# Performance work log

Hardware: AMD Instinct MI355X
Metric: run time of the kernel (lower is better)

Reference implementation:

```python
import jax, jax.numpy as jnp
import numpy as np

N, H, B, SS = 8192, 128, 64, 20


def _rate(z_a, z_b, k_idx, psi, W_om, b_om):
    # z_a, z_b: [..., H]; k_idx: int [...] event-type selector
    Wsel = W_om[k_idx]                    # [..., 2H]
    bsel = b_om[k_idx]
    psel = psi[k_idx]
    zab = jnp.concatenate([z_a, z_b], -1)
    zba = jnp.concatenate([z_b, z_a], -1)
    g = 0.5 * ((zab * Wsel).sum(-1) + bsel + (zba * Wsel).sum(-1) + bsel)
    x = jnp.clip(g / psel, -75.0, 75.0)
    return psel * jnp.log1p(jnp.exp(x))  # psi * log(1 + exp(g/psi))


def _forward(u, v, t, k, u_others, v_others, A, S, embeddings, last_event_time,
             W_S, W_R, W_t, W_h, b_h, psi, W_om, b_om):
    # 1) event intensities lambda_uvk  [B]
    lam = _rate(embeddings[u], embeddings[v], k, psi, W_om, b_om)
    # 2) survival loss. Replicates the original accumulation (incl. the
    #    v_surv = u_surv + rate_v overwrite bug): L_surv = sum_ev (2*(ru0+ru1)+rv1)/SS, shape [SS]
    z_u = embeddings[u][:, None, :]       # [B,1,H]
    z_v = embeddings[v][:, None, :]
    z_vo = embeddings[v_others]           # [B,SS,H]
    z_uo = embeddings[u_others]
    zub = jnp.broadcast_to(z_u, z_vo.shape)
    zvb = jnp.broadcast_to(z_v, z_uo.shape)
    k0 = jnp.zeros((B, SS), jnp.int32)
    k1 = jnp.ones((B, SS), jnp.int32)
    ru0 = _rate(zub, z_vo, k0, psi, W_om, b_om)
    ru1 = _rate(zub, z_vo, k1, psi, W_om, b_om)
    rv1 = _rate(zvb, z_uo, k1, psi, W_om, b_om)
    L_surv = (2.0 * (ru0 + ru1) + rv1).sum(0) / SS
    # 3) sequential per-event embedding update (the kernel-headroom part)
    def step(carry, ev):
        z, let = carry
        ui, vi, ti = ev
        h = z @ W_h.T + b_h               # [N,H] W_h applied to z_previous
        def side(n1, n2):
            dt = ti - let[n1]
            mask = A[n2] > 0              # neighbors of n2
            q = jnp.exp(S[n2]) * mask
            q = q / (q.sum() + 1e-7)
            vals = jnp.where(mask[:, None], jax.nn.sigmoid(q[:, None] * h), -jnp.inf)
            hs = jnp.where(mask.any(), vals.max(0), 0.0)   # max over neighbors
            return dt, hs
        dt0, hs0 = side(ui, vi)
        dt1, hs1 = side(vi, ui)
        dts = jnp.stack([dt0, dt1])       # [2]
        hstruct = jnp.stack([hs0, hs1])   # [2,H]
        L = hstruct @ W_S.T
        # original indexes z_prev[[n1,n2]] AFTER the inner loop, i.e. [v,u]
        rows = jnp.stack([vi, ui])
        Sterm = z[rows] @ W_R.T
        E = dts[:, None] * W_t[:, 0][None, :]   # Linear(1,H) on time deltas
        z = z.at[rows].set(jax.nn.sigmoid(L + Sterm + E))
        let = let.at[ui].set(ti).at[vi].set(ti)
        return (z, let), None
    (z_final, _), _ = jax.lax.scan(step, (embeddings, last_event_time), (u, v, t))
    return lam, L_surv, z_final


def setup_inputs():
    ks = jax.random.split(jax.random.key(0), 16)
    u = jax.random.randint(ks[0], (B,), 0, N)
    v = jax.random.randint(ks[1], (B,), 0, N)
    t = jnp.sort(jax.random.uniform(ks[2], (B,), jnp.float32) * 100.0)
    k = jax.random.randint(ks[3], (B,), 0, 2)
    u_others = jax.random.randint(ks[4], (B, SS), 0, N)
    v_others = jax.random.randint(ks[5], (B, SS), 0, N)
    Au = jax.random.uniform(ks[6], (N, N)) < (16.0 / N)   # avg degree ~16
    A = jnp.maximum(Au, Au.T).astype(jnp.float32)
    S = A / jnp.clip(A.sum(1, keepdims=True), 1.0)        # degree-normalized init
    embeddings = jax.random.uniform(ks[7], (N, H), jnp.float32)
    last_event_time = jnp.zeros((N,), jnp.float32)
    sc = 1.0 / np.sqrt(H)
    def lin(key, shape, s=sc):
        return jax.random.uniform(key, shape, jnp.float32, -s, s)
    W_S = lin(ks[8], (H, H)); W_R = lin(ks[9], (H, H))
    W_t = lin(ks[10], (H, 1)); W_h = lin(ks[11], (H, H)); b_h = lin(ks[12], (H,))
    psi = 0.5 * jnp.ones((2,), jnp.float32)
    sc2 = 1.0 / np.sqrt(2 * H)
    W_om = jax.random.uniform(ks[13], (2, 2 * H), jnp.float32, -sc2, sc2)
    b_om = jax.random.uniform(ks[14], (2,), jnp.float32, -sc2, sc2)
    return dict(u=u, v=v, t=t, k=k, u_others=u_others, v_others=v_others,
                A=A, S=S, embeddings=embeddings, last_event_time=last_event_time,
                W_S=W_S, W_R=W_R, W_t=W_t, W_h=W_h, b_h=b_h,
                psi=psi, W_om=W_om, b_om=b_om)


def reference(u, v, t, k, u_others, v_others, A, S, embeddings, last_event_time,
              W_S, W_R, W_t, W_h, b_h, psi, W_om, b_om):
    return _forward(u, v, t, k, u_others, v_others, A, S, embeddings, last_event_time,
                    W_S, W_R, W_t, W_h, b_h, psi, W_om, b_om)
```

## Files before the change

### kernel.cpp

```cpp
#include <hip/hip_runtime.h>
#include <math.h>

#define N 8192
#define H 128
#define NEV 64
#define SS 20
#define MAXD 512
#define MAXDIRTY 128
#define RPB 8
#define SPIN_GUARD (1 << 18)

__global__ __launch_bounds__(512) void k_emb(
    const float* __restrict__ emb, const float* __restrict__ W_h,
    const float* __restrict__ b_h, const float* __restrict__ W_om,
    float* __restrict__ h_tab, float* __restrict__ z_out,
    float* __restrict__ d0, float* __restrict__ d1,
    unsigned long long* __restrict__ donebits)
{
    const int tid = threadIdx.x;
    const int c = tid & 127;
    const int s = tid >> 7;
    const int r0 = blockIdx.x * RPB;

    if (blockIdx.x == 0 && tid == 0) donebits[0] = 0ull;

    __shared__ __align__(16) float z4[4 * 128];
    __shared__ float pr[16 * 128];

    float whr[32];
#pragma unroll
    for (int i = 0; i < 32; ++i) whr[i] = W_h[c * H + s * 32 + i];
    const float bh_c = b_h[c];

    const int lane = tid & 63;
    const int wid = tid >> 6;
    const int kof = (wid >= 4) ? 256 : 0;
    const float wk_l = W_om[kof + lane]      + W_om[kof + 128 + lane];
    const float wk_h = W_om[kof + 64 + lane] + W_om[kof + 192 + lane];

    for (int b = 0; b < RPB / 4; ++b) {
        const int rbase = r0 + b * 4;
        __syncthreads();
        const float zv = emb[(size_t)rbase * H + tid];
        z4[tid] = zv;
        z_out[(size_t)rbase * H + tid] = zv;
        __syncthreads();

#pragma unroll
        for (int rr = 0; rr < 4; ++rr) {
            float a = 0.f;
#pragma unroll
            for (int i4 = 0; i4 < 8; ++i4) {
                const float4 zz = *(const float4*)&z4[rr * 128 + s * 32 + i4 * 4];
                a += zz.x * whr[i4 * 4] + zz.y * whr[i4 * 4 + 1] +
                     zz.z * whr[i4 * 4 + 2] + zz.w * whr[i4 * 4 + 3];
            }
            pr[(s * 4 + rr) * 128 + c] = a;
        }
        {
            const int rr = wid & 3;
            float val = z4[rr * 128 + lane] * wk_l + z4[rr * 128 + 64 + lane] * wk_h;
#pragma unroll
            for (int off = 32; off > 0; off >>= 1) val += __shfl_xor(val, off);
            if (lane == 0) {
                if (wid < 4) d0[rbase + rr] = val;
                else         d1[rbase + rr] = val;
            }
        }
        __syncthreads();
        {
            const int rr = s;
            const float h = pr[(0 * 4 + rr) * 128 + c] + pr[(1 * 4 + rr) * 128 + c] +
                            pr[(2 * 4 + rr) * 128 + c] + pr[(3 * 4 + rr) * 128 + c] + bh_c;
            h_tab[(size_t)(rbase + rr) * H + c] = h;
        }
    }
}

__global__ __launch_bounds__(512) void k_parls(
    const int* __restrict__ u, const int* __restrict__ v,
    const float* __restrict__ t, const int* __restrict__ kk,
    const int* __restrict__ u_o, const int* __restrict__ v_o,
    const float* __restrict__ lastt, const float* __restrict__ emb,
    const float* __restrict__ A, const float* __restrict__ S,
    const float* __restrict__ h_tab,
    const float* __restrict__ W_S, const float* __restrict__ W_R,
    const float* __restrict__ W_t, const float* __restrict__ W_h,
    const float* __restrict__ b_h,
    const float* __restrict__ psi, const float* __restrict__ b_om,
    const float* __restrict__ d0, const float* __restrict__ d1,
    float* __restrict__ z_slot, float* __restrict__ h_slot,
    unsigned long long* __restrict__ donebits,
    float* __restrict__ lamout, float* __restrict__ svout,
    float* __restrict__ z_out)
{
    const int bid = blockIdx.x;
    const int tid = threadIdx.x;

    if (bid >= NEV) {
        if (bid == NEV) {
            if (tid < NEV) {
                const int b = tid;
                const int kv = kk[b];
                const float* dk = kv ? d1 : d0;
                const float g = 0.5f * (dk[u[b]] + dk[v[b]]) + b_om[kv];
                const float ps = psi[kv];
                const float x = fminf(75.f, fmaxf(-75.f, g / ps));
                lamout[b] = ps * log1pf(expf(x));
            }
        } else {
            const int s = bid - NEV - 1;
            if (tid < 64) {
                const int b = tid;
                const float p0 = psi[0], p1 = psi[1], bo0 = b_om[0], bo1 = b_om[1];
                const int vo = v_o[b * SS + s], uo = u_o[b * SS + s];
                float g, x;
                g = 0.5f * (d0[u[b]] + d0[vo]) + bo0; x = fminf(75.f, fmaxf(-75.f, g / p0));
                const float ru0 = p0 * log1pf(expf(x));
                g = 0.5f * (d1[u[b]] + d1[vo]) + bo1; x = fminf(75.f, fmaxf(-75.f, g / p1));
                const float ru1 = p1 * log1pf(expf(x));
                g = 0.5f * (d1[v[b]] + d1[uo]) + bo1; x = fminf(75.f, fmaxf(-75.f, g / p1));
                const float rv1 = p1 * log1pf(expf(x));
                float val = 2.f * (ru0 + ru1) + rv1;
#pragma unroll
                for (int off = 32; off > 0; off >>= 1) val += __shfl_xor(val, off);
                if (b == 0) svout[s] = val / (float)SS;
            }
        }
        return;
    }

    const int e = bid;
    const int r = (tid >> 7) & 1;
    const int c = tid & 127;
    const int slot = 2 * e + r;
    const int half = tid >> 8;
    const int ht = tid & 255;

    __shared__ int   uL[NEV], vL[NEV];
    __shared__ int   nbr2[2][MAXD];
    __shared__ float nbe2[2][MAXD];
    __shared__ int   flag2[2][MAXD];
    __shared__ float rs[512];
    __shared__ float redm[512];
    __shared__ float msA[2][128];
    __shared__ int   dlsA[2][MAXDIRTY];
    __shared__ float dlqA[2][MAXDIRTY];
    __shared__ int   dcA[2], degA[2], cntA[2];
    __shared__ float sumA[2];
    __shared__ __align__(16) float hs_s[2][128];
    __shared__ __align__(16) float zz_s[2][128];
    __shared__ __align__(16) float zn_s[2][128];
    __shared__ int   zdepL[2], lastupL[2], nodeL[2];
    __shared__ float dtvL[2];
    __shared__ unsigned long long maskN[4];
    __shared__ unsigned long long maskE[2];
    __shared__ unsigned long long need_s;

    if (tid < NEV)          uL[tid] = u[tid];
    else if (tid < 2 * NEV) vL[tid - NEV] = v[tid - NEV];
    if (tid < 2) { cntA[tid] = 0; dcA[tid] = 0; }
    __syncthreads();

    if (tid < 256) {
        const int i  = tid >> 7;
        const int hj = tid & 127;
        const int lane = tid & 63;
        const int w  = tid >> 6;
        const int node = i ? uL[e] : vL[e];
        const int dtn  = i ? vL[e] : uL[e];
        const bool m1 = (((hj & 1) ? uL[hj >> 1] : vL[hj >> 1]) == node);
        const unsigned long long b1 = __ballot(m1);
        if (lane == 0) maskN[w] = b1;
        const bool m2 = (uL[lane] == dtn) || (vL[lane] == dtn);
        const unsigned long long b2 = __ballot(m2);
        if (lane == 0 && (w & 1) == 0) maskE[i] = b2;
    }
    __syncthreads();
    if (tid < 2) {
        const int i = tid;
        const int sl = 2 * e + i;
        const int dtn = i ? vL[e] : uL[e];
        nodeL[i] = i ? uL[e] : vL[e];
        const unsigned long long lo = maskN[2 * i], hi = maskN[2 * i + 1];
        auto msk = [](int n) -> unsigned long long {
            return (n >= 64) ? ~0ull : ((n <= 0) ? 0ull : ((1ull << n) - 1ull));
        };
        const unsigned long long loB = lo & msk(2 * e);
        const unsigned long long hiB = hi & msk(2 * e - 64);
        int zd = -1;
        if (hiB)      zd = 64 + (63 - __builtin_clzll(hiB));
        else if (loB) zd = 63 - __builtin_clzll(loB);
        zdepL[i] = zd;
        const unsigned long long loA = lo & ~msk(sl + 1);
        const unsigned long long hiA = hi & ~msk(sl + 1 - 64);
        lastupL[i] = ((loA | hiA) == 0ull) ? 1 : 0;
        const unsigned long long me = maskE[i] & msk(e);
        const int pt = me ? (63 - __builtin_clzll(me)) : -1;
        const float lv = (pt >= 0) ? t[pt] : lastt[dtn];
        dtvL[i] = t[e] - lv;
    }
    __syncthreads();

    {
        const int rowN = half ? uL[e] : vL[e];
        const size_t baseN = (size_t)rowN * N;

        float lsum = 0.f;
        {
            const float4* A4 = (const float4*)(A + baseN);
            for (int j4 = ht; j4 < N / 4; j4 += 256) {
                const float4 a4 = A4[j4];
#pragma unroll
                for (int q = 0; q < 4; ++q) {
                    const float av = (q == 0) ? a4.x : (q == 1) ? a4.y
                                   : (q == 2) ? a4.z : a4.w;
                    if (av > 0.f) {
                        const int j = 4 * j4 + q;
                        const float ev = expf(S[baseN + j]);
                        lsum += ev;
                        const int p = atomicAdd(&cntA[half], 1);
                        if (p < MAXD) { nbr2[half][p] = j; nbe2[half][p] = ev; }
                    }
                }
            }
        }
        rs[tid] = lsum;
        __syncthreads();
        for (int off = 128; off > 0; off >>= 1) {
            if (ht < off) rs[tid] += rs[tid + off];
            __syncthreads();
        }
        if (ht == 0) { sumA[half] = rs[tid]; degA[half] = cntA[half]; }
        __syncthreads();

        const int dH = min(cntA[half], MAXD);
        const float rinvH = 1.f / (sumA[half] + 1e-7f);

        for (int j0 = ht; j0 < dH; j0 += 256) {
            const int j = nbr2[half][j0];
            int dep = -1;
            for (int s2 = 2 * e - 1; s2 >= 0; --s2) {
                const int nj = (s2 & 1) ? uL[s2 >> 1] : vL[s2 >> 1];
                if (nj == j) { dep = s2; break; }
            }
            flag2[half][j0] = dep;
        }
        __syncthreads();

        {
            const int cc = ht & 127, pr2 = ht >> 7;
            float m = -INFINITY;
            for (int j0 = pr2; j0 < dH; j0 += 2) {
                if (flag2[half][j0] < 0)
                    m = fmaxf(m, nbe2[half][j0] * rinvH *
                              h_tab[(size_t)nbr2[half][j0] * H + cc]);
            }
            redm[tid] = m;
            __syncthreads();
            if (ht < 128)
                msA[half][cc] = fmaxf(redm[half * 256 + cc],
                                      redm[half * 256 + 128 + cc]);
        }

        for (int j0 = ht; j0 < dH; j0 += 256) {
            const int dep = flag2[half][j0];
            if (dep >= 0) {
                const int p = atomicAdd(&dcA[half], 1);
                if (p < MAXDIRTY) { dlsA[half][p] = dep; dlqA[half][p] = nbe2[half][j0] * rinvH; }
            }
        }
        __syncthreads();
    }

    if (tid == 0) {
        unsigned long long need = 0ull;
        for (int rr = 0; rr < 2; ++rr) {
            const int zd = zdepL[rr];
            if (zd >= 0) need |= 1ull << (zd >> 1);
            const int dn = min(dcA[rr], MAXDIRTY);
            for (int p = 0; p < dn; ++p)
                need |= 1ull << (dlsA[rr][p] >> 1);
        }
        need_s = need;
        if (need) {
            int guard = 0;
            while ((__hip_atomic_load(donebits, __ATOMIC_ACQUIRE,
                                      __HIP_MEMORY_SCOPE_AGENT) & need) != need) {
                __builtin_amdgcn_s_sleep(2);
                if (++guard > SPIN_GUARD) break;
            }
        }
    }
    __syncthreads();
    if (need_s) {
        unsigned long long db = __hip_atomic_load(donebits, __ATOMIC_ACQUIRE,
                                                  __HIP_MEMORY_SCOPE_AGENT);
        (void)db;
    }

    if (tid < 256) {
        float m = msA[r][c];
        const int dn = min(dcA[r], MAXDIRTY);
        for (int p = 0; p < dn; ++p) {
            const int ds = dlsA[r][p];
            const float q = dlqA[r][p];
            m = fmaxf(m, q * h_slot[ds * H + c]);
        }
        hs_s[r][c] = (degA[r] > 0) ? 1.f / (1.f + __expf(-m)) : 0.f;
        const int zd = zdepL[r];
        zz_s[r][c] = (zd >= 0) ? z_slot[zd * H + c]
                               : emb[(size_t)nodeL[r] * H + c];
    }
    __syncthreads();

    if (tid < 256) {
        float g = 0.f;
        const float4* ws4 = (const float4*)(W_S + (size_t)c * H);
        const float4* wr4 = (const float4*)(W_R + (size_t)c * H);
#pragma unroll
        for (int i = 0; i < 32; ++i) {
            const float4 a = ws4[i];
            const float4 b = wr4[i];
            const float4 hh = *(const float4*)&hs_s[r][4 * i];
            const float4 zz = *(const float4*)&zz_s[r][4 * i];
            g += hh.x * a.x + hh.y * a.y + hh.z * a.z + hh.w * a.w +
                 zz.x * b.x + zz.y * b.y + zz.z * b.z + zz.w * b.w;
        }
        g += dtvL[r] * W_t[c];
        const float zv = 1.f / (1.f + __expf(-g));
        zn_s[r][c] = zv;
        z_slot[slot * H + c] = zv;
        if (lastupL[r])
            z_out[(size_t)nodeL[r] * H + c] = zv;
    }
    __syncthreads();

    if (tid < 256) {
        float h = 0.f;
        const float4* wh4 = (const float4*)(W_h + (size_t)c * H);
#pragma unroll
        for (int i = 0; i < 32; ++i) {
            const float4 a = wh4[i];
            const float4 zz = *(const float4*)&zn_s[r][4 * i];
            h += zz.x * a.x + zz.y * a.y + zz.z * a.z + zz.w * a.w;
        }
        h_slot[slot * H + c] = h + b_h[c];
    }

    __syncthreads();
    if (tid == 0) {
        __threadfence();
        __hip_atomic_fetch_or(donebits, 1ull << e, __ATOMIC_RELEASE,
                              __HIP_MEMORY_SCOPE_AGENT);
    }
}

extern "C" void kernel_launch(void* const* d_in, const int* in_sizes, int n_in,
                              void* d_out, int out_size, void* d_ws, size_t ws_size,
                              hipStream_t stream)
{
    const int*   u        = (const int*)d_in[0];
    const int*   v        = (const int*)d_in[1];
    const float* t        = (const float*)d_in[2];
    const int*   k        = (const int*)d_in[3];
    const int*   u_others = (const int*)d_in[4];
    const int*   v_others = (const int*)d_in[5];
    const float* A        = (const float*)d_in[6];
    const float* S        = (const float*)d_in[7];
    const float* emb      = (const float*)d_in[8];
    const float* lastt    = (const float*)d_in[9];
    const float* W_S      = (const float*)d_in[10];
    const float* W_R      = (const float*)d_in[11];
    const float* W_t      = (const float*)d_in[12];
    const float* W_h      = (const float*)d_in[13];
    const float* b_h      = (const float*)d_in[14];
    const float* psi      = (const float*)d_in[15];
    const float* W_om     = (const float*)d_in[16];
    const float* b_om     = (const float*)d_in[17];
    (void)in_sizes; (void)n_in; (void)out_size; (void)ws_size;

    float* wsf    = (float*)d_ws;
    float* h_tab  = wsf;
    float* d0     = h_tab + (size_t)N * H;
    float* d1     = d0 + N;
    float* Mstat  = d1 + N;
    float* dl_q   = Mstat + 128 * H;
    float* z_slot = dl_q + 128 * MAXDIRTY;
    float* h_slot = z_slot + 128 * H;
    int*   deg    = (int*)(h_slot + 128 * H);
    int*   dcnt   = deg + 128;
    int*   dl_s   = dcnt + 128;
    unsigned long long* donebits = (unsigned long long*)(dl_s + 128 * MAXDIRTY);

    float* out    = (float*)d_out;
    float* lamout = out;
    float* svout  = out + NEV;
    float* z_out  = out + NEV + SS;

    k_emb<<<N / RPB, 512, 0, stream>>>(emb, W_h, b_h, W_om, h_tab, z_out,
                                       d0, d1, donebits);
    k_parls<<<NEV + 1 + SS, 512, 0, stream>>>(u, v, t, k, u_others, v_others,
                                              lastt, emb, A, S, h_tab,
                                              W_S, W_R, W_t, W_h, b_h,
                                              psi, b_om, d0, d1,
                                              z_slot, h_slot, donebits,
                                              lamout, svout, z_out);
}
```

Before: 87.03 us.

## Fuse embedding and event kernels into one launch with counter-based dependency

Merges the embedding/h-table kernel and the per-event kernel into one grid. Embedding blocks bump a global atomic counter when they finish. Lambda and survival blocks spin on that counter before reading d0/d1, while the event blocks do their neighbor setup first and wait only before reading h_tab. This overlaps the event preamble with the embedding pass and removes a kernel launch boundary. The rows handled per embedding block are doubled, and a small memset now resets the counters each call. The risks are spin-wait deadlock if the event blocks are scheduled ahead of embedding blocks, and the fact that SPIN_GUARD can break out early, which would leave correctness at risk.

```diff
diff --git a/kernel.cpp b/kernel.cpp
--- a/kernel.cpp
+++ b/kernel.cpp
@@ -7,136 +7,37 @@
 #define SS 20
 #define MAXD 512
 #define MAXDIRTY 128
-#define RPB 8
+#define RPB 16
 #define SPIN_GUARD (1 << 18)
 
-__global__ __launch_bounds__(512) void k_emb(
-    const float* __restrict__ emb, const float* __restrict__ W_h,
-    const float* __restrict__ b_h, const float* __restrict__ W_om,
-    float* __restrict__ h_tab, float* __restrict__ z_out,
-    float* __restrict__ d0, float* __restrict__ d1,
-    unsigned long long* __restrict__ donebits)
-{
-    const int tid = threadIdx.x;
-    const int c = tid & 127;
-    const int s = tid >> 7;
-    const int r0 = blockIdx.x * RPB;
-
-    if (blockIdx.x == 0 && tid == 0) donebits[0] = 0ull;
-
-    __shared__ __align__(16) float z4[4 * 128];
-    __shared__ float pr[16 * 128];
-
-    float whr[32];
-#pragma unroll
-    for (int i = 0; i < 32; ++i) whr[i] = W_h[c * H + s * 32 + i];
-    const float bh_c = b_h[c];
-
-    const int lane = tid & 63;
-    const int wid = tid >> 6;
-    const int kof = (wid >= 4) ? 256 : 0;
-    const float wk_l = W_om[kof + lane]      + W_om[kof + 128 + lane];
-    const float wk_h = W_om[kof + 64 + lane] + W_om[kof + 192 + lane];
-
-    for (int b = 0; b < RPB / 4; ++b) {
-        const int rbase = r0 + b * 4;
-        __syncthreads();
-        const float zv = emb[(size_t)rbase * H + tid];
-        z4[tid] = zv;
-        z_out[(size_t)rbase * H + tid] = zv;
-        __syncthreads();
-
-#pragma unroll
-        for (int rr = 0; rr < 4; ++rr) {
-            float a = 0.f;
-#pragma unroll
-            for (int i4 = 0; i4 < 8; ++i4) {
-                const float4 zz = *(const float4*)&z4[rr * 128 + s * 32 + i4 * 4];
-                a += zz.x * whr[i4 * 4] + zz.y * whr[i4 * 4 + 1] +
-                     zz.z * whr[i4 * 4 + 2] + zz.w * whr[i4 * 4 + 3];
-            }
-            pr[(s * 4 + rr) * 128 + c] = a;
-        }
-        {
-            const int rr = wid & 3;
-            float val = z4[rr * 128 + lane] * wk_l + z4[rr * 128 + 64 + lane] * wk_h;
-#pragma unroll
-            for (int off = 32; off > 0; off >>= 1) val += __shfl_xor(val, off);
-            if (lane == 0) {
-                if (wid < 4) d0[rbase + rr] = val;
-                else         d1[rbase + rr] = val;
-            }
-        }
-        __syncthreads();
-        {
-            const int rr = s;
-            const float h = pr[(0 * 4 + rr) * 128 + c] + pr[(1 * 4 + rr) * 128 + c] +
-                            pr[(2 * 4 + rr) * 128 + c] + pr[(3 * 4 + rr) * 128 + c] + bh_c;
-            h_tab[(size_t)(rbase + rr) * H + c] = h;
-        }
-    }
-}
-
-__global__ __launch_bounds__(512) void k_parls(
+#define EMB_BLOCKS (N / RPB)
+#define LAM_BID    EMB_BLOCKS
+#define SURV_BID0  (LAM_BID + 1)
+#define PAR_BID0   (SURV_BID0 + SS)
+#define GRID_ALL   (PAR_BID0 + NEV)
+#define C_EMB_TARGET EMB_BLOCKS
+
+__global__ __launch_bounds__(512) void k_all(
     const int* __restrict__ u, const int* __restrict__ v,
     const float* __restrict__ t, const int* __restrict__ kk,
     const int* __restrict__ u_o, const int* __restrict__ v_o,
     const float* __restrict__ lastt, const float* __restrict__ emb,
     const float* __restrict__ A, const float* __restrict__ S,
-    const float* __restrict__ h_tab,
     const float* __restrict__ W_S, const float* __restrict__ W_R,
     const float* __restrict__ W_t, const float* __restrict__ W_h,
-    const float* __restrict__ b_h,
+    const float* __restrict__ b_h, const float* __restrict__ W_om,
     const float* __restrict__ psi, const float* __restrict__ b_om,
-    const float* __restrict__ d0, const float* __restrict__ d1,
+    float* __restrict__ h_tab, float* __restrict__ d0, float* __restrict__ d1,
     float* __restrict__ z_slot, float* __restrict__ h_slot,
-    unsigned long long* __restrict__ donebits,
+    unsigned long long* __restrict__ donebits, int* __restrict__ c_emb,
     float* __restrict__ lamout, float* __restrict__ svout,
     float* __restrict__ z_out)
 {
     const int bid = blockIdx.x;
     const int tid = threadIdx.x;
 
-    if (bid >= NEV) {
-        if (bid == NEV) {
-            if (tid < NEV) {
-                const int b = tid;
-                const int kv = kk[b];
-                const float* dk = kv ? d1 : d0;
-                const float g = 0.5f * (dk[u[b]] + dk[v[b]]) + b_om[kv];
-                const float ps = psi[kv];
-                const float x = fminf(75.f, fmaxf(-75.f, g / ps));
-                lamout[b] = ps * log1pf(expf(x));
-            }
-        } else {
-            const int s = bid - NEV - 1;
-            if (tid < 64) {
-                const int b = tid;
-                const float p0 = psi[0], p1 = psi[1], bo0 = b_om[0], bo1 = b_om[1];
-                const int vo = v_o[b * SS + s], uo = u_o[b * SS + s];
-                float g, x;
-                g = 0.5f * (d0[u[b]] + d0[vo]) + bo0; x = fminf(75.f, fmaxf(-75.f, g / p0));
-                const float ru0 = p0 * log1pf(expf(x));
-                g = 0.5f * (d1[u[b]] + d1[vo]) + bo1; x = fminf(75.f, fmaxf(-75.f, g / p1));
-                const float ru1 = p1 * log1pf(expf(x));
-                g = 0.5f * (d1[v[b]] + d1[uo]) + bo1; x = fminf(75.f, fmaxf(-75.f, g / p1));
-                const float rv1 = p1 * log1pf(expf(x));
-                float val = 2.f * (ru0 + ru1) + rv1;
-#pragma unroll
-                for (int off = 32; off > 0; off >>= 1) val += __shfl_xor(val, off);
-                if (b == 0) svout[s] = val / (float)SS;
-            }
-        }
-        return;
-    }
-
-    const int e = bid;
-    const int r = (tid >> 7) & 1;
-    const int c = tid & 127;
-    const int slot = 2 * e + r;
-    const int half = tid >> 8;
-    const int ht = tid & 255;
-
+    __shared__ __align__(16) float z4[4 * 128];
+    __shared__ float pr[16 * 128];
     __shared__ int   uL[NEV], vL[NEV];
     __shared__ int   nbr2[2][MAXD];
     __shared__ float nbe2[2][MAXD];
@@ -156,6 +57,120 @@
     __shared__ unsigned long long maskN[4];
     __shared__ unsigned long long maskE[2];
     __shared__ unsigned long long need_s;
+
+    if (bid < EMB_BLOCKS) {
+        const int c = tid & 127;
+        const int s = tid >> 7;
+        const int r0 = bid * RPB;
+
+        float whr[32];
+#pragma unroll
+        for (int i = 0; i < 32; ++i) whr[i] = W_h[c * H + s * 32 + i];
+        const float bh_c = b_h[c];
+
+        const int lane = tid & 63;
+        const int wid = tid >> 6;
+        const int kof = (wid >= 4) ? 256 : 0;
+        const float wk_l = W_om[kof + lane]      + W_om[kof + 128 + lane];
+        const float wk_h = W_om[kof + 64 + lane] + W_om[kof + 192 + lane];
+
+        for (int b = 0; b < RPB / 4; ++b) {
+            const int rbase = r0 + b * 4;
+            __syncthreads();
+            const float zv = emb[(size_t)rbase * H + tid];
+            z4[tid] = zv;
+            z_out[(size_t)rbase * H + tid] = zv;
+            __syncthreads();
+
+#pragma unroll
+            for (int rr = 0; rr < 4; ++rr) {
+                float a = 0.f;
+#pragma unroll
+                for (int i4 = 0; i4 < 8; ++i4) {
+                    const float4 zz = *(const float4*)&z4[rr * 128 + s * 32 + i4 * 4];
+                    a += zz.x * whr[i4 * 4] + zz.y * whr[i4 * 4 + 1] +
+                         zz.z * whr[i4 * 4 + 2] + zz.w * whr[i4 * 4 + 3];
+                }
+                pr[(s * 4 + rr) * 128 + c] = a;
+            }
+            {
+                const int rr = wid & 3;
+                float val = z4[rr * 128 + lane] * wk_l + z4[rr * 128 + 64 + lane] * wk_h;
+#pragma unroll
+                for (int off = 32; off > 0; off >>= 1) val += __shfl_xor(val, off);
+                if (lane == 0) {
+                    if (wid < 4) d0[rbase + rr] = val;
+                    else         d1[rbase + rr] = val;
+                }
+            }
+            __syncthreads();
+            {
+                const int rr = s;
+                const float h = pr[(0 * 4 + rr) * 128 + c] + pr[(1 * 4 + rr) * 128 + c] +
+                                pr[(2 * 4 + rr) * 128 + c] + pr[(3 * 4 + rr) * 128 + c] + bh_c;
+                h_tab[(size_t)(rbase + rr) * H + c] = h;
+            }
+        }
+        __syncthreads();
+        if (tid == 0) {
+            __threadfence();
+            __hip_atomic_fetch_add(c_emb, 1, __ATOMIC_RELEASE,
+                                   __HIP_MEMORY_SCOPE_AGENT);
+        }
+        return;
+    }
+
+    if (bid < PAR_BID0) {
+        if (tid == 0) {
+            int guard = 0;
+            while (__hip_atomic_load(c_emb, __ATOMIC_ACQUIRE,
+                                     __HIP_MEMORY_SCOPE_AGENT) < C_EMB_TARGET) {
+                __builtin_amdgcn_s_sleep(2);
+                if (++guard > SPIN_GUARD) break;
+            }
+        }
+        __syncthreads();
+        { int x = __hip_atomic_load(c_emb, __ATOMIC_ACQUIRE,
+                                    __HIP_MEMORY_SCOPE_AGENT); (void)x; }
+
+        if (bid == LAM_BID) {
+            if (tid < NEV) {
+                const int b = tid;
+                const int kv = kk[b];
+                const float* dk = kv ? d1 : d0;
+                const float g = 0.5f * (dk[u[b]] + dk[v[b]]) + b_om[kv];
+                const float ps = psi[kv];
+                const float x = fminf(75.f, fmaxf(-75.f, g / ps));
+                lamout[b] = ps * log1pf(expf(x));
+            }
+        } else {
+            const int s = bid - SURV_BID0;
+            if (tid < 64) {
+                const int b = tid;
+                const float p0 = psi[0], p1 = psi[1], bo0 = b_om[0], bo1 = b_om[1];
+                const int vo = v_o[b * SS + s], uo = u_o[b * SS + s];
+                float g, x;
+                g = 0.5f * (d0[u[b]] + d0[vo]) + bo0; x = fminf(75.f, fmaxf(-75.f, g / p0));
+                const float ru0 = p0 * log1pf(expf(x));
+                g = 0.5f * (d1[u[b]] + d1[vo]) + bo1; x = fminf(75.f, fmaxf(-75.f, g / p1));
+                const float ru1 = p1 * log1pf(expf(x));
+                g = 0.5f * (d1[v[b]] + d1[uo]) + bo1; x = fminf(75.f, fmaxf(-75.f, g / p1));
+                const float rv1 = p1 * log1pf(expf(x));
+                float val = 2.f * (ru0 + ru1) + rv1;
+#pragma unroll
+                for (int off = 32; off > 0; off >>= 1) val += __shfl_xor(val, off);
+                if (b == 0) svout[s] = val / (float)SS;
+            }
+        }
+        return;
+    }
+
+    const int e = bid - PAR_BID0;
+    const int r = (tid >> 7) & 1;
+    const int c = tid & 127;
+    const int slot = 2 * e + r;
+    const int half = tid >> 8;
+    const int ht = tid & 255;
 
     if (tid < NEV)          uL[tid] = u[tid];
     else if (tid < 2 * NEV) vL[tid - NEV] = v[tid - NEV];
@@ -247,6 +262,18 @@
             flag2[half][j0] = dep;
         }
         __syncthreads();
+
+        if (tid == 0) {
+            int guard = 0;
+            while (__hip_atomic_load(c_emb, __ATOMIC_ACQUIRE,
+                                     __HIP_MEMORY_SCOPE_AGENT) < C_EMB_TARGET) {
+                __builtin_amdgcn_s_sleep(2);
+                if (++guard > SPIN_GUARD) break;
+            }
+        }
+        __syncthreads();
+        { int x = __hip_atomic_load(c_emb, __ATOMIC_ACQUIRE,
+                                    __HIP_MEMORY_SCOPE_AGENT); (void)x; }
 
         {
             const int cc = ht & 127, pr2 = ht >> 7;
@@ -380,30 +407,25 @@
     const float* b_om     = (const float*)d_in[17];
     (void)in_sizes; (void)n_in; (void)out_size; (void)ws_size;
 
-    float* wsf    = (float*)d_ws;
-    float* h_tab  = wsf;
+    unsigned long long* donebits = (unsigned long long*)d_ws;
+    int*   c_emb  = (int*)(donebits + 1);
+    float* h_tab  = (float*)d_ws + 4;
     float* d0     = h_tab + (size_t)N * H;
     float* d1     = d0 + N;
-    float* Mstat  = d1 + N;
-    float* dl_q   = Mstat + 128 * H;
-    float* z_slot = dl_q + 128 * MAXDIRTY;
+    float* z_slot = d1 + N;
     float* h_slot = z_slot + 128 * H;
-    int*   deg    = (int*)(h_slot + 128 * H);
-    int*   dcnt   = deg + 128;
-    int*   dl_s   = dcnt + 128;
-    unsigned long long* donebits = (unsigned long long*)(dl_s + 128 * MAXDIRTY);
 
     float* out    = (float*)d_out;
     float* lamout = out;
     float* svout  = out + NEV;
     float* z_out  = out + NEV + SS;
 
-    k_emb<<<N / RPB, 512, 0, stream>>>(emb, W_h, b_h, W_om, h_tab, z_out,
-                                       d0, d1, donebits);
-    k_parls<<<NEV + 1 + SS, 512, 0, stream>>>(u, v, t, k, u_others, v_others,
-                                              lastt, emb, A, S, h_tab,
-                                              W_S, W_R, W_t, W_h, b_h,
-                                              psi, b_om, d0, d1,
-                                              z_slot, h_slot, donebits,
-                                              lamout, svout, z_out);
+    hipMemsetAsync(d_ws, 0, 16, stream);
+    k_all<<<GRID_ALL, 512, 0, stream>>>(u, v, t, k, u_others, v_others,
+                                        lastt, emb, A, S,
+                                        W_S, W_R, W_t, W_h, b_h, W_om,
+                                        psi, b_om,
+                                        h_tab, d0, d1, z_slot, h_slot,
+                                        donebits, c_emb,
+                                        lamout, svout, z_out);
 }
```

Measured after the change: 114.6 us. 1.32x slower.

## Move embedding copy to extra blocks in second kernel, overlapping the event loop

Applied to the files above, without the earlier changes.

The copy of embeddings into the output moves out of the first kernel into 256 extra blocks of the second kernel. Those blocks signal completion through an atomic counter, which event blocks wait on before their writeback phase. The goal is to shorten the first kernel and overlap the 4 MB copy with the event work. The cost is an added memset launch, an extra spin-wait, and possible contention if the copy blocks take compute units needed by the event blocks.

```diff
diff --git a/kernel.cpp b/kernel.cpp
--- a/kernel.cpp
+++ b/kernel.cpp
@@ -10,11 +10,13 @@
 #define RPB 8
 #define SPIN_GUARD (1 << 18)
 
+#define CPY_BLOCKS 256
+#define PAR_GRID   (NEV + 1 + SS + CPY_BLOCKS)
+
 __global__ __launch_bounds__(512) void k_emb(
     const float* __restrict__ emb, const float* __restrict__ W_h,
     const float* __restrict__ b_h, const float* __restrict__ W_om,
-    float* __restrict__ h_tab, float* __restrict__ z_out,
-    float* __restrict__ d0, float* __restrict__ d1,
+    float* __restrict__ h_tab, float* __restrict__ d0, float* __restrict__ d1,
     unsigned long long* __restrict__ donebits)
 {
     const int tid = threadIdx.x;
@@ -41,9 +43,7 @@
     for (int b = 0; b < RPB / 4; ++b) {
         const int rbase = r0 + b * 4;
         __syncthreads();
-        const float zv = emb[(size_t)rbase * H + tid];
-        z4[tid] = zv;
-        z_out[(size_t)rbase * H + tid] = zv;
+        z4[tid] = emb[(size_t)rbase * H + tid];
         __syncthreads();
 
 #pragma unroll
@@ -90,12 +90,28 @@
     const float* __restrict__ psi, const float* __restrict__ b_om,
     const float* __restrict__ d0, const float* __restrict__ d1,
     float* __restrict__ z_slot, float* __restrict__ h_slot,
-    unsigned long long* __restrict__ donebits,
+    unsigned long long* __restrict__ donebits, int* __restrict__ c_cpy,
     float* __restrict__ lamout, float* __restrict__ svout,
     float* __restrict__ z_out)
 {
     const int bid = blockIdx.x;
     const int tid = threadIdx.x;
+
+    if (bid >= NEV + 1 + SS) {
+        const int cb = bid - (NEV + 1 + SS);
+        const size_t total = (size_t)N * H;
+        const size_t per = total / CPY_BLOCKS;
+        const float4* src = (const float4*)(emb + cb * per);
+        float4* dst = (float4*)(z_out + cb * per);
+        for (size_t i = tid; i < per / 4; i += 512) dst[i] = src[i];
+        __syncthreads();
+        if (tid == 0) {
+            __threadfence();
+            __hip_atomic_fetch_add(c_cpy, 1, __ATOMIC_RELEASE,
+                                   __HIP_MEMORY_SCOPE_AGENT);
+        }
+        return;
+    }
 
     if (bid >= NEV) {
         if (bid == NEV) {
@@ -272,6 +288,18 @@
         }
         __syncthreads();
     }
+
+    if (tid == 0) {
+        int guard = 0;
+        while (__hip_atomic_load(c_cpy, __ATOMIC_ACQUIRE,
+                                 __HIP_MEMORY_SCOPE_AGENT) < CPY_BLOCKS) {
+            __builtin_amdgcn_s_sleep(2);
+            if (++guard > SPIN_GUARD) break;
+        }
+    }
+    __syncthreads();
+    { int x = __hip_atomic_load(c_cpy, __ATOMIC_ACQUIRE,
+                                __HIP_MEMORY_SCOPE_AGENT); (void)x; }
 
     if (tid == 0) {
         unsigned long long need = 0ull;
@@ -380,30 +408,25 @@
     const float* b_om     = (const float*)d_in[17];
     (void)in_sizes; (void)n_in; (void)out_size; (void)ws_size;
 
-    float* wsf    = (float*)d_ws;
-    float* h_tab  = wsf;
+    unsigned long long* donebits = (unsigned long long*)d_ws;
+    int*   c_cpy  = (int*)(donebits + 1);
+    float* h_tab  = (float*)d_ws + 4;
     float* d0     = h_tab + (size_t)N * H;
     float* d1     = d0 + N;
-    float* Mstat  = d1 + N;
-    float* dl_q   = Mstat + 128 * H;
-    float* z_slot = dl_q + 128 * MAXDIRTY;
+    float* z_slot = d1 + N;
     float* h_slot = z_slot + 128 * H;
-    int*   deg    = (int*)(h_slot + 128 * H);
-    int*   dcnt   = deg + 128;
-    int*   dl_s   = dcnt + 128;
-    unsigned long long* donebits = (unsigned long long*)(dl_s + 128 * MAXDIRTY);
 
     float* out    = (float*)d_out;
     float* lamout = out;
     float* svout  = out + NEV;
     float* z_out  = out + NEV + SS;
 
-    k_emb<<<N / RPB, 512, 0, stream>>>(emb, W_h, b_h, W_om, h_tab, z_out,
-                                       d0, d1, donebits);
-    k_parls<<<NEV + 1 + SS, 512, 0, stream>>>(u, v, t, k, u_others, v_others,
-                                              lastt, emb, A, S, h_tab,
-                                              W_S, W_R, W_t, W_h, b_h,
-                                              psi, b_om, d0, d1,
-                                              z_slot, h_slot, donebits,
-                                              lamout, svout, z_out);
+    hipMemsetAsync(d_ws, 0, 16, stream);
+    k_emb<<<N / RPB, 512, 0, stream>>>(emb, W_h, b_h, W_om, h_tab, d0, d1, donebits);
+    k_parls<<<PAR_GRID, 512, 0, stream>>>(u, v, t, k, u_others, v_others,
+                                          lastt, emb, A, S, h_tab,
+                                          W_S, W_R, W_t, W_h, b_h,
+                                          psi, b_om, d0, d1,
+                                          z_slot, h_slot, donebits, c_cpy,
+                                          lamout, svout, z_out);
 }
```

Result: slower. 101.4 us (+16.5%).
